# Optimization experiments

Measured on AMD Instinct MI355X. Metric: run time of the kernel, lower is better.

## Reference

```python
import jax, jax.numpy as jnp
import numpy as np

N = 100000
E = 1000000
D = 64


def setup_inputs() -> dict:
    key = jax.random.key(0)
    k1, k2, k3 = jax.random.split(key, 3)
    x = jax.random.normal(k1, (N, D), dtype=jnp.float32)
    edge_index = jax.random.randint(k2, (2, E), 0, N, dtype=jnp.int64)
    W = jax.random.normal(k3, (D, D), dtype=jnp.float32) * (1.0 / np.sqrt(D))  # nn.Linear weight [out, in]
    return {"x": x, "edge_index": edge_index, "W": W, "num_nodes": N}


def reference(x, edge_index, W, num_nodes):
    src, dst = edge_index[0], edge_index[1]
    # in-degree (counted on dst) + self loop
    deg = jnp.zeros((num_nodes,), dtype=x.dtype).at[dst].add(1.0) + 1.0
    dis = deg ** -0.5  # deg^{-1/2}, shape [N]
    # gather src features, scale by deg_inv_sqrt[src], scatter-add to dst
    msg = x[src] * dis[src][:, None]  # [E, D]
    agg = jnp.zeros_like(x).at[dst].add(msg)  # [N, D]
    # self-loop contribution, then scale by deg_inv_sqrt on the node axis
    agg = (agg + x * dis[:, None]) * dis[:, None]
    # linear (no bias): agg @ W^T with W of shape [out, in]
    return agg @ W.T
```

## Files before the change

### kernel.cpp

```cpp
#include <hip/hip_runtime.h>

#define FD 64

typedef __attribute__((ext_vector_type(8))) short bf16x8;
typedef __attribute__((ext_vector_type(4))) float f32x4;
typedef __attribute__((ext_vector_type(4))) unsigned short u16x4;

__device__ inline short f2bf(float f) {
    union { float f; unsigned u; } v; v.f = f;
    unsigned r = (v.u + 0x7fffu + ((v.u >> 16) & 1u)) >> 16;
    return (short)r;
}
__device__ inline float bf2f(unsigned short u) {
    union { unsigned u; float f; } v; v.u = ((unsigned)u) << 16;
    return v.f;
}

__global__ void degpos_kernel(const int* __restrict__ dst, int* __restrict__ degi,
                              unsigned short* __restrict__ pos, int E) {
    int i = blockIdx.x * blockDim.x + threadIdx.x;
    int stride = gridDim.x * blockDim.x;
    for (; i < E; i += stride) {
        pos[i] = (unsigned short)atomicAdd(&degi[dst[i]], 1);
    }
}

#define SCAN_ELEMS 2048

__global__ void scan1_kernel(const int* __restrict__ degi, int* __restrict__ offs,
                             int* __restrict__ bsums, float* __restrict__ dis, int N) {
    __shared__ int tsum[256];
    int base = blockIdx.x * SCAN_ELEMS + threadIdx.x * 8;
    int v[8];
    int s = 0;
    #pragma unroll
    for (int k = 0; k < 8; ++k) {
        int idx = base + k;
        v[k] = (idx < N) ? degi[idx] : 0;
        if (idx < N) dis[idx] = rsqrtf((float)v[k] + 1.0f);
        s += v[k];
    }
    tsum[threadIdx.x] = s;
    __syncthreads();
    for (int off = 1; off < 256; off <<= 1) {
        int t = (threadIdx.x >= off) ? tsum[threadIdx.x - off] : 0;
        __syncthreads();
        tsum[threadIdx.x] += t;
        __syncthreads();
    }
    int excl = (threadIdx.x == 0) ? 0 : tsum[threadIdx.x - 1];
    #pragma unroll
    for (int k = 0; k < 8; ++k) {
        int idx = base + k;
        if (idx < N) offs[idx] = excl;
        excl += v[k];
    }
    if (threadIdx.x == 255) bsums[blockIdx.x] = tsum[255];
}

__global__ void scan2_kernel(int* __restrict__ bsums, int nb) {
    __shared__ int t[256];
    int v = (threadIdx.x < nb) ? bsums[threadIdx.x] : 0;
    t[threadIdx.x] = v;
    __syncthreads();
    for (int off = 1; off < 256; off <<= 1) {
        int u = (threadIdx.x >= off) ? t[threadIdx.x - off] : 0;
        __syncthreads();
        t[threadIdx.x] += u;
        __syncthreads();
    }
    if (threadIdx.x < nb) bsums[threadIdx.x] = (threadIdx.x == 0) ? 0 : t[threadIdx.x - 1];
}

__global__ void scan3_kernel(int* __restrict__ offs, const int* __restrict__ bsums, int N) {
    int i = blockIdx.x * blockDim.x + threadIdx.x;
    if (i < N) offs[i] += bsums[i / SCAN_ELEMS];
}

__global__ void fill_pos_kernel(const int* __restrict__ src, const int* __restrict__ dst,
                                const int* __restrict__ offs, const int* __restrict__ bsums,
                                const unsigned short* __restrict__ pos,
                                int* __restrict__ bucket, int E) {
    int i = blockIdx.x * blockDim.x + threadIdx.x;
    int stride = gridDim.x * blockDim.x;
    for (; i < E; i += stride) {
        int d = dst[i];
        bucket[offs[d] + bsums[d >> 11] + (int)pos[i]] = src[i];
    }
}

__global__ __launch_bounds__(256) void z_mfma_kernel(
        const float* __restrict__ x, const float* __restrict__ dis,
        const float* __restrict__ W, unsigned short* __restrict__ z, int N) {
    int lane = threadIdx.x & 63;
    int r16  = lane & 15;
    int kg   = lane >> 4;

    bf16x8 bfrag[4][2];
    #pragma unroll
    for (int ct = 0; ct < 4; ++ct) {
        #pragma unroll
        for (int kk = 0; kk < 2; ++kk) {
            const float* wp = W + (size_t)(ct * 16 + r16) * FD + kk * 32 + kg * 8;
            float4 w0 = *(const float4*)wp;
            float4 w1 = *(const float4*)(wp + 4);
            bf16x8 b;
            b[0] = f2bf(w0.x); b[1] = f2bf(w0.y); b[2] = f2bf(w0.z); b[3] = f2bf(w0.w);
            b[4] = f2bf(w1.x); b[5] = f2bf(w1.y); b[6] = f2bf(w1.z); b[7] = f2bf(w1.w);
            bfrag[ct][kk] = b;
        }
    }

    int wid    = blockIdx.x * (blockDim.x >> 6) + (threadIdx.x >> 6);
    int nwaves = gridDim.x * (blockDim.x >> 6);
    int tiles  = (N + 15) >> 4;

    for (int t = wid; t < tiles; t += nwaves) {
        int n0  = t << 4;
        int row = n0 + r16;
        int rl  = row < N ? row : N - 1;
        const float* xp = x + (size_t)rl * FD + kg * 8;
        float4 a00 = *(const float4*)(xp);
        float4 a01 = *(const float4*)(xp + 4);
        float4 a10 = *(const float4*)(xp + 32);
        float4 a11 = *(const float4*)(xp + 36);
        bf16x8 a0, a1;
        a0[0] = f2bf(a00.x); a0[1] = f2bf(a00.y); a0[2] = f2bf(a00.z); a0[3] = f2bf(a00.w);
        a0[4] = f2bf(a01.x); a0[5] = f2bf(a01.y); a0[6] = f2bf(a01.z); a0[7] = f2bf(a01.w);
        a1[0] = f2bf(a10.x); a1[1] = f2bf(a10.y); a1[2] = f2bf(a10.z); a1[3] = f2bf(a10.w);
        a1[4] = f2bf(a11.x); a1[5] = f2bf(a11.y); a1[6] = f2bf(a11.z); a1[7] = f2bf(a11.w);

        f32x4 acc[4];
        #pragma unroll
        for (int ct = 0; ct < 4; ++ct) {
            acc[ct] = (f32x4){0.f, 0.f, 0.f, 0.f};
            acc[ct] = __builtin_amdgcn_mfma_f32_16x16x32_bf16(a0, bfrag[ct][0], acc[ct], 0, 0, 0);
            acc[ct] = __builtin_amdgcn_mfma_f32_16x16x32_bf16(a1, bfrag[ct][1], acc[ct], 0, 0, 0);
        }

        #pragma unroll
        for (int reg = 0; reg < 4; ++reg) {
            int nr = n0 + kg * 4 + reg;
            if (nr < N) {
                float dn = dis[nr];
                #pragma unroll
                for (int ct = 0; ct < 4; ++ct) {
                    z[(size_t)nr * FD + ct * 16 + r16] =
                        (unsigned short)f2bf(acc[ct][reg] * dn);
                }
            }
        }
    }
}

__global__ __launch_bounds__(256) void gather_z_kernel(
        const unsigned short* __restrict__ z, const int* __restrict__ offs,
        const int* __restrict__ bsums, const int* __restrict__ degi,
        const int* __restrict__ bucket, const float* __restrict__ dis,
        float* __restrict__ out, int N) {
    int wave = threadIdx.x >> 6;
    int lane = threadIdx.x & 63;
    int n = blockIdx.x * 4 + wave;
    if (n >= N) return;

    int g  = lane >> 4;
    int fl = lane & 15;
    unsigned fo = (unsigned)(fl << 2);

    int j   = offs[n] + bsums[n >> 11];
    int end = j + degi[n];

    float4 acc = make_float4(0.f, 0.f, 0.f, 0.f);

    for (; j + 8 <= end; j += 8) {
        int4 b0 = *(const int4*)&bucket[j];
        int4 b1 = *(const int4*)&bucket[j + 4];
        int s0 = (g & 2) ? ((g & 1) ? b0.w : b0.z) : ((g & 1) ? b0.y : b0.x);
        int s1 = (g & 2) ? ((g & 1) ? b1.w : b1.z) : ((g & 1) ? b1.y : b1.x);
        u16x4 r0 = *(const u16x4*)(z + (((unsigned)s0 << 6) | fo));
        u16x4 r1 = *(const u16x4*)(z + (((unsigned)s1 << 6) | fo));
        acc.x += bf2f(r0[0]) + bf2f(r1[0]);
        acc.y += bf2f(r0[1]) + bf2f(r1[1]);
        acc.z += bf2f(r0[2]) + bf2f(r1[2]);
        acc.w += bf2f(r0[3]) + bf2f(r1[3]);
    }
    for (; j + 4 <= end; j += 4) {
        int4 b = *(const int4*)&bucket[j];
        int s = (g & 2) ? ((g & 1) ? b.w : b.z) : ((g & 1) ? b.y : b.x);
        u16x4 r = *(const u16x4*)(z + (((unsigned)s << 6) | fo));
        acc.x += bf2f(r[0]);
        acc.y += bf2f(r[1]);
        acc.z += bf2f(r[2]);
        acc.w += bf2f(r[3]);
    }
    if (j < end) {
        int rem = end - j;
        if (g < rem) {
            int s = bucket[j + g];
            u16x4 r = *(const u16x4*)(z + (((unsigned)s << 6) | fo));
            acc.x += bf2f(r[0]);
            acc.y += bf2f(r[1]);
            acc.z += bf2f(r[2]);
            acc.w += bf2f(r[3]);
        }
    }
    if (g == 0) {
        u16x4 r = *(const u16x4*)(z + (((unsigned)n << 6) | fo));
        acc.x += bf2f(r[0]);
        acc.y += bf2f(r[1]);
        acc.z += bf2f(r[2]);
        acc.w += bf2f(r[3]);
    }

    acc.x += __shfl_xor(acc.x, 32, 64);
    acc.y += __shfl_xor(acc.y, 32, 64);
    acc.z += __shfl_xor(acc.z, 32, 64);
    acc.w += __shfl_xor(acc.w, 32, 64);
    acc.x += __shfl_xor(acc.x, 16, 64);
    acc.y += __shfl_xor(acc.y, 16, 64);
    acc.z += __shfl_xor(acc.z, 16, 64);
    acc.w += __shfl_xor(acc.w, 16, 64);

    if (g == 0) {
        float dn = dis[n];
        float4 o = make_float4(acc.x * dn, acc.y * dn, acc.z * dn, acc.w * dn);
        *(float4*)(out + (size_t)n * FD + fo) = o;
    }
}

__global__ void deg_kernel(const int* __restrict__ dst, int* __restrict__ degi, int E) {
    int i = blockIdx.x * blockDim.x + threadIdx.x;
    int stride = gridDim.x * blockDim.x;
    for (; i < E; i += stride) {
        atomicAdd(&degi[dst[i]], 1);
    }
}

__global__ void fill_kernel(const int* __restrict__ src, const int* __restrict__ dst,
                            const int* __restrict__ offs, int* __restrict__ cursor,
                            int* __restrict__ bucket, int E) {
    int i = blockIdx.x * blockDim.x + threadIdx.x;
    int stride = gridDim.x * blockDim.x;
    for (; i < E; i += stride) {
        int d = dst[i];
        int p = atomicAdd(&cursor[d], 1);
        bucket[offs[d] + p] = src[i];
    }
}

__global__ __launch_bounds__(256) void gather_linear_kernel(
        const float* __restrict__ x, const int* __restrict__ offs,
        const int* __restrict__ degi, const int* __restrict__ bucket,
        const float* __restrict__ dis, const float* __restrict__ W,
        float* __restrict__ out, int N) {
    __shared__ float Wt[FD][FD + 1];
    __shared__ float rows[4][FD];

    for (int t = threadIdx.x; t < FD * FD; t += 256) {
        Wt[t & 63][t >> 6] = W[t];
    }
    __syncthreads();

    int wave = threadIdx.x >> 6;
    int lane = threadIdx.x & 63;
    int n = blockIdx.x * 4 + wave;

    if (n < N) {
        int j   = offs[n];
        int end = j + degi[n];
        float acc = 0.0f;
        for (; j + 3 < end; j += 4) {
            int s0 = bucket[j], s1 = bucket[j + 1], s2 = bucket[j + 2], s3 = bucket[j + 3];
            float d0 = dis[s0], d1 = dis[s1], d2 = dis[s2], d3 = dis[s3];
            float v0 = x[(size_t)s0 * FD + lane];
            float v1 = x[(size_t)s1 * FD + lane];
            float v2 = x[(size_t)s2 * FD + lane];
            float v3 = x[(size_t)s3 * FD + lane];
            acc += v0 * d0 + v1 * d1 + v2 * d2 + v3 * d3;
        }
        for (; j < end; ++j) {
            int s = bucket[j];
            acc += x[(size_t)s * FD + lane] * dis[s];
        }
        float dn = dis[n];
        rows[wave][lane] = (acc + x[(size_t)n * FD + lane] * dn) * dn;
    }
    if (n < N) {
        float o = 0.0f;
        #pragma unroll
        for (int i = 0; i < FD; i += 4) {
            float4 r = *(const float4*)&rows[wave][i];
            o += r.x * Wt[i + 0][lane]
               + r.y * Wt[i + 1][lane]
               + r.z * Wt[i + 2][lane]
               + r.w * Wt[i + 3][lane];
        }
        out[(size_t)n * FD + lane] = o;
    }
}

extern "C" void kernel_launch(void* const* d_in, const int* in_sizes, int n_in,
                              void* d_out, int out_size, void* d_ws, size_t ws_size,
                              hipStream_t stream) {
    const float* x  = (const float*)d_in[0];
    const int*   ei = (const int*)d_in[1];
    const float* W  = (const float*)d_in[2];

    const int N = in_sizes[0] / FD;
    const int E = in_sizes[1] / 2;
    const int* src = ei;
    const int* dst = ei + E;

    float* out = (float*)d_out;
    const int nb = (N + SCAN_ELEMS - 1) / SCAN_ELEMS;

    size_t posB = (((size_t)E * 2) + 3) & ~(size_t)3;
    size_t need_full = ((size_t)N * 3 + 1024 + (size_t)E) * 4 + posB + (size_t)N * FD * 2;

    if (ws_size >= need_full) {
        char* ws = (char*)d_ws;
        int*   degi   = (int*)ws;    ws += (size_t)N * 4;
        float* dis    = (float*)ws;  ws += (size_t)N * 4;
        int*   offs   = (int*)ws;    ws += (size_t)N * 4;
        int*   bsums  = (int*)ws;    ws += 1024 * 4;
        int*   bucket = (int*)ws;    ws += (size_t)E * 4;
        unsigned short* pos = (unsigned short*)ws;  ws += posB;
        unsigned short* z   = (unsigned short*)ws;

        hipMemsetAsync(degi, 0, (size_t)N * 4, stream);
        degpos_kernel<<<2048, 256, 0, stream>>>(dst, degi, pos, E);
        scan1_kernel<<<nb, 256, 0, stream>>>(degi, offs, bsums, dis, N);
        scan2_kernel<<<1, 256, 0, stream>>>(bsums, nb);
        z_mfma_kernel<<<512, 256, 0, stream>>>(x, dis, W, z, N);
        fill_pos_kernel<<<2048, 256, 0, stream>>>(src, dst, offs, bsums, pos, bucket, E);
        gather_z_kernel<<<(N + 3) / 4, 256, 0, stream>>>(z, offs, bsums, degi, bucket, dis, out, N);
    } else {
        char* ws = (char*)d_ws;
        int*   degi   = (int*)ws;    ws += (size_t)N * 4;
        float* dis    = (float*)ws;  ws += (size_t)N * 4;
        int*   offs   = (int*)ws;    ws += (size_t)N * 4;
        int*   cursor = (int*)ws;    ws += (size_t)N * 4;
        int*   bsums  = (int*)ws;    ws += 1024 * 4;
        int*   bucket = (int*)ws;

        hipMemsetAsync(degi,   0, (size_t)N * 4, stream);
        hipMemsetAsync(cursor, 0, (size_t)N * 4, stream);
        deg_kernel<<<2048, 256, 0, stream>>>(dst, degi, E);
        scan1_kernel<<<nb, 256, 0, stream>>>(degi, offs, bsums, dis, N);
        scan2_kernel<<<1, 256, 0, stream>>>(bsums, nb);
        scan3_kernel<<<(N + 255) / 256, 256, 0, stream>>>(offs, bsums, N);
        fill_kernel<<<2048, 256, 0, stream>>>(src, dst, offs, cursor, bucket, E);
        gather_linear_kernel<<<(N + 3) / 4, 256, 0, stream>>>(
            x, offs, degi, bucket, dis, W, out, N);
    }
}
```

Measured before the change: 138.4 us.

## Slice z into four 16-column planes and gather one plane per block

Stores the transformed features z as four slice-major planes of 16 columns instead of row-major 64-wide rows. The gather kernel now uses a fixed grid with a grid-stride loop, and each block handles only one slice, chosen from the low bits of the block id. The goal is to shrink the randomly accessed working set per block, and likely per XCD given round-robin block placement, so each slice stays resident in L2. The cost is four times the bucket index reads, narrower 2-byte loads per lane, and narrower scattered output stores.

```diff
diff --git a/kernel.cpp b/kernel.cpp
--- a/kernel.cpp
+++ b/kernel.cpp
@@ -4,7 +4,6 @@
 
 typedef __attribute__((ext_vector_type(8))) short bf16x8;
 typedef __attribute__((ext_vector_type(4))) float f32x4;
-typedef __attribute__((ext_vector_type(4))) unsigned short u16x4;
 
 __device__ inline short f2bf(float f) {
     union { float f; unsigned u; } v; v.f = f;
@@ -145,86 +144,64 @@
                 float dn = dis[nr];
                 #pragma unroll
                 for (int ct = 0; ct < 4; ++ct) {
-                    z[(size_t)nr * FD + ct * 16 + r16] =
+                    z[((size_t)ct * N + nr) * 16 + r16] =
                         (unsigned short)f2bf(acc[ct][reg] * dn);
                 }
             }
         }
     }
 }
+
+#define GATHER_BLOCKS 16384
 
 __global__ __launch_bounds__(256) void gather_z_kernel(
         const unsigned short* __restrict__ z, const int* __restrict__ offs,
         const int* __restrict__ bsums, const int* __restrict__ degi,
         const int* __restrict__ bucket, const float* __restrict__ dis,
         float* __restrict__ out, int N) {
-    int wave = threadIdx.x >> 6;
-    int lane = threadIdx.x & 63;
-    int n = blockIdx.x * 4 + wave;
-    if (n >= N) return;
-
+    int slice  = blockIdx.x & 3;
+    int bchunk = blockIdx.x >> 2;
+    int wave   = threadIdx.x >> 6;
+    int lane   = threadIdx.x & 63;
     int g  = lane >> 4;
     int fl = lane & 15;
-    unsigned fo = (unsigned)(fl << 2);
-
-    int j   = offs[n] + bsums[n >> 11];
-    int end = j + degi[n];
-
-    float4 acc = make_float4(0.f, 0.f, 0.f, 0.f);
-
-    for (; j + 8 <= end; j += 8) {
-        int4 b0 = *(const int4*)&bucket[j];
-        int4 b1 = *(const int4*)&bucket[j + 4];
-        int s0 = (g & 2) ? ((g & 1) ? b0.w : b0.z) : ((g & 1) ? b0.y : b0.x);
-        int s1 = (g & 2) ? ((g & 1) ? b1.w : b1.z) : ((g & 1) ? b1.y : b1.x);
-        u16x4 r0 = *(const u16x4*)(z + (((unsigned)s0 << 6) | fo));
-        u16x4 r1 = *(const u16x4*)(z + (((unsigned)s1 << 6) | fo));
-        acc.x += bf2f(r0[0]) + bf2f(r1[0]);
-        acc.y += bf2f(r0[1]) + bf2f(r1[1]);
-        acc.z += bf2f(r0[2]) + bf2f(r1[2]);
-        acc.w += bf2f(r0[3]) + bf2f(r1[3]);
-    }
-    for (; j + 4 <= end; j += 4) {
-        int4 b = *(const int4*)&bucket[j];
-        int s = (g & 2) ? ((g & 1) ? b.w : b.z) : ((g & 1) ? b.y : b.x);
-        u16x4 r = *(const u16x4*)(z + (((unsigned)s << 6) | fo));
-        acc.x += bf2f(r[0]);
-        acc.y += bf2f(r[1]);
-        acc.z += bf2f(r[2]);
-        acc.w += bf2f(r[3]);
-    }
-    if (j < end) {
-        int rem = end - j;
-        if (g < rem) {
-            int s = bucket[j + g];
-            u16x4 r = *(const u16x4*)(z + (((unsigned)s << 6) | fo));
-            acc.x += bf2f(r[0]);
-            acc.y += bf2f(r[1]);
-            acc.z += bf2f(r[2]);
-            acc.w += bf2f(r[3]);
-        }
-    }
-    if (g == 0) {
-        u16x4 r = *(const u16x4*)(z + (((unsigned)n << 6) | fo));
-        acc.x += bf2f(r[0]);
-        acc.y += bf2f(r[1]);
-        acc.z += bf2f(r[2]);
-        acc.w += bf2f(r[3]);
-    }
-
-    acc.x += __shfl_xor(acc.x, 32, 64);
-    acc.y += __shfl_xor(acc.y, 32, 64);
-    acc.z += __shfl_xor(acc.z, 32, 64);
-    acc.w += __shfl_xor(acc.w, 32, 64);
-    acc.x += __shfl_xor(acc.x, 16, 64);
-    acc.y += __shfl_xor(acc.y, 16, 64);
-    acc.z += __shfl_xor(acc.z, 16, 64);
-    acc.w += __shfl_xor(acc.w, 16, 64);
-
-    if (g == 0) {
-        float dn = dis[n];
-        float4 o = make_float4(acc.x * dn, acc.y * dn, acc.z * dn, acc.w * dn);
-        *(float4*)(out + (size_t)n * FD + fo) = o;
+
+    const unsigned short* zs = z + (size_t)slice * N * 16;
+
+    for (int n = bchunk * 4 + wave; n < N; n += GATHER_BLOCKS) {
+        int j   = offs[n] + bsums[n >> 11];
+        int end = j + degi[n];
+
+        float acc = 0.0f;
+
+        for (; j + 8 <= end; j += 8) {
+            int4 b0 = *(const int4*)&bucket[j];
+            int4 b1 = *(const int4*)&bucket[j + 4];
+            int s0 = (g & 2) ? ((g & 1) ? b0.w : b0.z) : ((g & 1) ? b0.y : b0.x);
+            int s1 = (g & 2) ? ((g & 1) ? b1.w : b1.z) : ((g & 1) ? b1.y : b1.x);
+            acc += bf2f(zs[((unsigned)s0 << 4) | fl]);
+            acc += bf2f(zs[((unsigned)s1 << 4) | fl]);
+        }
+        for (; j + 4 <= end; j += 4) {
+            int4 b = *(const int4*)&bucket[j];
+            int s = (g & 2) ? ((g & 1) ? b.w : b.z) : ((g & 1) ? b.y : b.x);
+            acc += bf2f(zs[((unsigned)s << 4) | fl]);
+        }
+        if (j < end) {
+            int rem = end - j;
+            if (g < rem) {
+                int s = bucket[j + g];
+                acc += bf2f(zs[((unsigned)s << 4) | fl]);
+            }
+        }
+
+        acc += __shfl_xor(acc, 32, 64);
+        acc += __shfl_xor(acc, 16, 64);
+
+        if (g == 0) {
+            float v = (acc + bf2f(zs[((unsigned)n << 4) | fl])) * dis[n];
+            out[(size_t)n * FD + slice * 16 + fl] = v;
+        }
     }
 }
 
@@ -333,7 +310,7 @@
         scan2_kernel<<<1, 256, 0, stream>>>(bsums, nb);
         z_mfma_kernel<<<512, 256, 0, stream>>>(x, dis, W, z, N);
         fill_pos_kernel<<<2048, 256, 0, stream>>>(src, dst, offs, bsums, pos, bucket, E);
-        gather_z_kernel<<<(N + 3) / 4, 256, 0, stream>>>(z, offs, bsums, degi, bucket, dis, out, N);
+        gather_z_kernel<<<GATHER_BLOCKS, 256, 0, stream>>>(z, offs, bsums, degi, bucket, dis, out, N);
     } else {
         char* ws = (char*)d_ws;
         int*   degi   = (int*)ws;    ws += (size_t)N * 4;
```

After: 217.1 us. 56.8% more time.
